# Kernel optimization log

Measured on AMD Instinct MI355X. Metric: run time of the kernel, lower is better.

Reference implementation:

```python
import jax, jax.numpy as jnp
import numpy as np

TEMPERATURE = 3.0
SINKHORN_ITERS = 20
NOISE_SCALE = 1.0
EPS = 1e-20


def setup_inputs() -> dict:
    key = jax.random.key(0)
    k1, k2, k3 = jax.random.split(key, 3)
    x = jax.random.normal(k1, (524288, 128), dtype=jnp.float32)
    logits = jax.random.normal(k2, (128, 128), dtype=jnp.float32)
    u = jax.random.uniform(k3, (128, 128), dtype=jnp.float32)
    return {"x": x, "logits": logits, "u": u}


def reference(x, logits, u):
    # Gumbel noise from uniform sample (matches sample_gumbel)
    gumbel = -jnp.log(-jnp.log(u + EPS) + EPS) * NOISE_SCALE
    log_alpha = (logits + gumbel) / TEMPERATURE
    log_alpha = jnp.clip(log_alpha, -10.0, 10.0)
    A = jnp.exp(log_alpha)
    # Sinkhorn: alternate row / column normalization (fixed 20 iters)
    for _ in range(SINKHORN_ITERS):
        A = A / jnp.sum(A, axis=1, keepdims=True)
        A = A / jnp.sum(A, axis=0, keepdims=True)
    P = jnp.nan_to_num(A, nan=0.0, posinf=1.0, neginf=0.0)
    # [batch, num_inputs] @ [num_inputs, num_leaves]
    return x @ P.T
```

## Files before the change

kernel.cpp:

```cpp
#include <hip/hip_runtime.h>
#include <hip/hip_bf16.h>

typedef _Float16 half8 __attribute__((ext_vector_type(8)));
typedef float floatx4 __attribute__((ext_vector_type(4)));

__global__ __launch_bounds__(128, 1) void sinkhorn128(
    const float* __restrict__ logits, const float* __restrict__ u,
    _Float16* __restrict__ Pout) {
    __shared__ float sA[128 * 129];
    __shared__ alignas(16) float sVec[128];
    const int i = threadIdx.x;

    float a0[128];
    float a0t[128];

    #pragma unroll
    for (int j = 0; j < 128; ++j) {
        float lg = logits[i * 128 + j];
        float uu = u[i * 128 + j];
        float g  = -logf(-logf(uu + 1e-20f) + 1e-20f);
        float la = (lg + g) / 3.0f;
        la = fminf(10.0f, fmaxf(-10.0f, la));
        float a = expf(la);
        a0[j] = a;
        sA[i * 129 + j] = a;
    }
    sVec[i] = 1.0f;
    __syncthreads();
    #pragma unroll
    for (int j = 0; j < 128; ++j) a0t[j] = sA[j * 129 + i];

    float ri = 1.0f;
    for (int it = 0; it < 20; ++it) {
        float s0 = 0.f, s1 = 0.f, s2 = 0.f, s3 = 0.f;
        #pragma unroll
        for (int j = 0; j < 128; j += 4) {
            float4 c4 = *reinterpret_cast<const float4*>(&sVec[j]);
            s0 = fmaf(a0[j + 0], c4.x, s0);
            s1 = fmaf(a0[j + 1], c4.y, s1);
            s2 = fmaf(a0[j + 2], c4.z, s2);
            s3 = fmaf(a0[j + 3], c4.w, s3);
        }
        ri = 1.0f / ((s0 + s1) + (s2 + s3));
        __syncthreads();
        sVec[i] = ri;
        __syncthreads();
        s0 = s1 = s2 = s3 = 0.f;
        #pragma unroll
        for (int j = 0; j < 128; j += 4) {
            float4 r4 = *reinterpret_cast<const float4*>(&sVec[j]);
            s0 = fmaf(a0t[j + 0], r4.x, s0);
            s1 = fmaf(a0t[j + 1], r4.y, s1);
            s2 = fmaf(a0t[j + 2], r4.z, s2);
            s3 = fmaf(a0t[j + 3], r4.w, s3);
        }
        float ci = 1.0f / ((s0 + s1) + (s2 + s3));
        __syncthreads();
        sVec[i] = ci;
        __syncthreads();
    }

    #pragma unroll
    for (int j = 0; j < 128; j += 2) {
        union { _Float16 h[2]; unsigned int w; } pk;
        pk.h[0] = (_Float16)(ri * a0[j + 0] * sVec[j + 0]);
        pk.h[1] = (_Float16)(ri * a0[j + 1] * sVec[j + 1]);
        reinterpret_cast<unsigned int*>(Pout)[(i * 128 + j) >> 1] = pk.w;
    }
}

__global__ __launch_bounds__(256, 2) void streamMatmul(
    const float* __restrict__ x, const _Float16* __restrict__ P,
    float* __restrict__ out) {
    const int lane = threadIdx.x & 63;
    const int wv   = threadIdx.x >> 6;
    const int gw   = blockIdx.x * 4 + wv;
    const int r    = lane & 15;
    const int q    = lane >> 4;

    half8 Bf[4][8];
    #pragma unroll
    for (int ks = 0; ks < 4; ++ks)
        #pragma unroll
        for (int nt = 0; nt < 8; ++nt)
            Bf[ks][nt] = *reinterpret_cast<const half8*>(
                P + (nt * 16 + r) * 128 + ks * 32 + q * 8);

    const long baseRow = (long)gw * 256;
    for (int t = 0; t < 16; ++t) {
        const long m0 = baseRow + t * 16;
        const float* xp = x + (m0 + r) * 128 + q * 8;

        floatx4 xa[4][2];
        #pragma unroll
        for (int ks = 0; ks < 4; ++ks) {
            xa[ks][0] = __builtin_nontemporal_load(
                reinterpret_cast<const floatx4*>(xp + ks * 32));
            xa[ks][1] = __builtin_nontemporal_load(
                reinterpret_cast<const floatx4*>(xp + ks * 32 + 4));
        }

        floatx4 acc[8];
        #pragma unroll
        for (int nt = 0; nt < 8; ++nt) acc[nt] = (floatx4){0.f, 0.f, 0.f, 0.f};

        #pragma unroll
        for (int ks = 0; ks < 4; ++ks) {
            half8 ahi, alo;
            #pragma unroll
            for (int jj = 0; jj < 8; ++jj) {
                float f = (jj < 4) ? xa[ks][0][jj] : xa[ks][1][jj - 4];
                _Float16 h = (_Float16)f;
                ahi[jj] = h;
                alo[jj] = (_Float16)(f - (float)h);
            }
            #pragma unroll
            for (int nt = 0; nt < 8; ++nt) {
                acc[nt] = __builtin_amdgcn_mfma_f32_16x16x32_f16(
                    ahi, Bf[ks][nt], acc[nt], 0, 0, 0);
                acc[nt] = __builtin_amdgcn_mfma_f32_16x16x32_f16(
                    alo, Bf[ks][nt], acc[nt], 0, 0, 0);
            }
        }

        float* op = out + (m0 + q * 4) * 128 + r;
        #pragma unroll
        for (int nt = 0; nt < 8; ++nt)
            #pragma unroll
            for (int rr = 0; rr < 4; ++rr)
                __builtin_nontemporal_store(acc[nt][rr], op + rr * 128 + nt * 16);
    }
}

extern "C" void kernel_launch(void* const* d_in, const int* in_sizes, int n_in,
                              void* d_out, int out_size, void* d_ws, size_t ws_size,
                              hipStream_t stream) {
    (void)in_sizes; (void)n_in; (void)out_size; (void)ws_size;
    const float* x      = (const float*)d_in[0];
    const float* logits = (const float*)d_in[1];
    const float* u      = (const float*)d_in[2];
    float* out          = (float*)d_out;
    _Float16* P         = (_Float16*)d_ws;

    sinkhorn128<<<1, 128, 0, stream>>>(logits, u, P);
    streamMatmul<<<512, 256, 0, stream>>>(x, P, out);
}
```

Measured before the change: 534.0 us.

## Split Sinkhorn row/column work across 256 threads and double-buffer x loads

The Sinkhorn kernel now runs 256 threads, with one half owning rows and the other half owning columns, so each thread keeps a single 128-float register array instead of two. The initialisation is spread across all threads and uses fast __logf/__expf intrinsics. The matmul kernel prefetches the next 16-row x tile into a second register buffer while computing the current one, to hide global load latency. Costs are higher register pressure in the matmul kernel and slightly less accurate transcendentals in the Sinkhorn prologue.

```diff
diff --git a/kernel.cpp b/kernel.cpp
--- a/kernel.cpp
+++ b/kernel.cpp
@@ -4,68 +4,79 @@
 typedef _Float16 half8 __attribute__((ext_vector_type(8)));
 typedef float floatx4 __attribute__((ext_vector_type(4)));
 
-__global__ __launch_bounds__(128, 1) void sinkhorn128(
+__global__ __launch_bounds__(256, 1) void sinkhorn128(
     const float* __restrict__ logits, const float* __restrict__ u,
     _Float16* __restrict__ Pout) {
     __shared__ float sA[128 * 129];
-    __shared__ alignas(16) float sVec[128];
-    const int i = threadIdx.x;
+    __shared__ alignas(16) float sC[128];
+    __shared__ alignas(16) float sR[128];
+    const int t = threadIdx.x;
+    const bool isRow = t < 128;
+    const int idx = t & 127;
 
-    float a0[128];
-    float a0t[128];
+    #pragma unroll 4
+    for (int j = 0; j < 64; ++j) {
+        const int f = t * 64 + j;
+        float lg = logits[f];
+        float uu = u[f];
+        float g  = -__logf(-__logf(uu + 1e-20f) + 1e-20f);
+        float la = (lg + g) * (1.0f / 3.0f);
+        la = fminf(10.0f, fmaxf(-10.0f, la));
+        sA[(f >> 7) * 129 + (f & 127)] = __expf(la);
+    }
+    if (t < 128) sC[t] = 1.0f;
+    __syncthreads();
 
-    #pragma unroll
-    for (int j = 0; j < 128; ++j) {
-        float lg = logits[i * 128 + j];
-        float uu = u[i * 128 + j];
-        float g  = -logf(-logf(uu + 1e-20f) + 1e-20f);
-        float la = (lg + g) / 3.0f;
-        la = fminf(10.0f, fmaxf(-10.0f, la));
-        float a = expf(la);
-        a0[j] = a;
-        sA[i * 129 + j] = a;
+    float av[128];
+    if (isRow) {
+        #pragma unroll
+        for (int j = 0; j < 128; ++j) av[j] = sA[idx * 129 + j];
+    } else {
+        #pragma unroll
+        for (int j = 0; j < 128; ++j) av[j] = sA[j * 129 + idx];
     }
-    sVec[i] = 1.0f;
-    __syncthreads();
-    #pragma unroll
-    for (int j = 0; j < 128; ++j) a0t[j] = sA[j * 129 + i];
 
     float ri = 1.0f;
+    #pragma unroll 1
     for (int it = 0; it < 20; ++it) {
-        float s0 = 0.f, s1 = 0.f, s2 = 0.f, s3 = 0.f;
-        #pragma unroll
-        for (int j = 0; j < 128; j += 4) {
-            float4 c4 = *reinterpret_cast<const float4*>(&sVec[j]);
-            s0 = fmaf(a0[j + 0], c4.x, s0);
-            s1 = fmaf(a0[j + 1], c4.y, s1);
-            s2 = fmaf(a0[j + 2], c4.z, s2);
-            s3 = fmaf(a0[j + 3], c4.w, s3);
+        if (isRow) {
+            float s0 = 0.f, s1 = 0.f, s2 = 0.f, s3 = 0.f;
+            #pragma unroll
+            for (int j = 0; j < 128; j += 4) {
+                float4 c4 = *reinterpret_cast<const float4*>(&sC[j]);
+                s0 = fmaf(av[j + 0], c4.x, s0);
+                s1 = fmaf(av[j + 1], c4.y, s1);
+                s2 = fmaf(av[j + 2], c4.z, s2);
+                s3 = fmaf(av[j + 3], c4.w, s3);
+            }
+            ri = 1.0f / ((s0 + s1) + (s2 + s3));
         }
-        ri = 1.0f / ((s0 + s1) + (s2 + s3));
         __syncthreads();
-        sVec[i] = ri;
+        if (isRow) sR[idx] = ri;
         __syncthreads();
-        s0 = s1 = s2 = s3 = 0.f;
-        #pragma unroll
-        for (int j = 0; j < 128; j += 4) {
-            float4 r4 = *reinterpret_cast<const float4*>(&sVec[j]);
-            s0 = fmaf(a0t[j + 0], r4.x, s0);
-            s1 = fmaf(a0t[j + 1], r4.y, s1);
-            s2 = fmaf(a0t[j + 2], r4.z, s2);
-            s3 = fmaf(a0t[j + 3], r4.w, s3);
+        if (!isRow) {
+            float s0 = 0.f, s1 = 0.f, s2 = 0.f, s3 = 0.f;
+            #pragma unroll
+            for (int j = 0; j < 128; j += 4) {
+                float4 r4 = *reinterpret_cast<const float4*>(&sR[j]);
+                s0 = fmaf(av[j + 0], r4.x, s0);
+                s1 = fmaf(av[j + 1], r4.y, s1);
+                s2 = fmaf(av[j + 2], r4.z, s2);
+                s3 = fmaf(av[j + 3], r4.w, s3);
+            }
+            sC[idx] = 1.0f / ((s0 + s1) + (s2 + s3));
         }
-        float ci = 1.0f / ((s0 + s1) + (s2 + s3));
-        __syncthreads();
-        sVec[i] = ci;
         __syncthreads();
     }
 
-    #pragma unroll
-    for (int j = 0; j < 128; j += 2) {
-        union { _Float16 h[2]; unsigned int w; } pk;
-        pk.h[0] = (_Float16)(ri * a0[j + 0] * sVec[j + 0]);
-        pk.h[1] = (_Float16)(ri * a0[j + 1] * sVec[j + 1]);
-        reinterpret_cast<unsigned int*>(Pout)[(i * 128 + j) >> 1] = pk.w;
+    if (isRow) {
+        #pragma unroll
+        for (int j = 0; j < 128; j += 2) {
+            union { _Float16 h[2]; unsigned int w; } pk;
+            pk.h[0] = (_Float16)(ri * av[j + 0] * sC[j + 0]);
+            pk.h[1] = (_Float16)(ri * av[j + 1] * sC[j + 1]);
+            reinterpret_cast<unsigned int*>(Pout)[(idx * 128 + j) >> 1] = pk.w;
+        }
     }
 }
 
@@ -87,11 +98,12 @@
                 P + (nt * 16 + r) * 128 + ks * 32 + q * 8);
 
     const long baseRow = (long)gw * 256;
-    for (int t = 0; t < 16; ++t) {
-        const long m0 = baseRow + t * 16;
-        const float* xp = x + (m0 + r) * 128 + q * 8;
+    const float* xbase = x + (baseRow + r) * 128 + q * 8;
 
-        floatx4 xa[4][2];
+    floatx4 xa0[4][2], xa1[4][2];
+
+    auto issue = [&](int t, floatx4 (&xa)[4][2]) {
+        const float* xp = xbase + (long)t * (16 * 128);
         #pragma unroll
         for (int ks = 0; ks < 4; ++ks) {
             xa[ks][0] = __builtin_nontemporal_load(
@@ -99,11 +111,12 @@
             xa[ks][1] = __builtin_nontemporal_load(
                 reinterpret_cast<const floatx4*>(xp + ks * 32 + 4));
         }
+    };
 
+    auto compute_store = [&](int t, floatx4 (&xa)[4][2]) {
         floatx4 acc[8];
         #pragma unroll
         for (int nt = 0; nt < 8; ++nt) acc[nt] = (floatx4){0.f, 0.f, 0.f, 0.f};
-
         #pragma unroll
         for (int ks = 0; ks < 4; ++ks) {
             half8 ahi, alo;
@@ -122,13 +135,22 @@
                     alo, Bf[ks][nt], acc[nt], 0, 0, 0);
             }
         }
-
-        float* op = out + (m0 + q * 4) * 128 + r;
+        float* op = out + (baseRow + t * 16 + q * 4) * 128 + r;
         #pragma unroll
         for (int nt = 0; nt < 8; ++nt)
             #pragma unroll
             for (int rr = 0; rr < 4; ++rr)
-                __builtin_nontemporal_store(acc[nt][rr], op + rr * 128 + nt * 16);
+                __builtin_nontemporal_store(acc[nt][rr],
+                                            op + rr * 128 + nt * 16);
+    };
+
+    issue(0, xa0);
+    #pragma unroll 1
+    for (int t = 0; t < 16; t += 2) {
+        issue(t + 1, xa1);
+        compute_store(t, xa0);
+        if (t + 2 < 16) issue(t + 2, xa0);
+        compute_store(t + 1, xa1);
     }
 }
 
@@ -142,6 +164,6 @@
     float* out          = (float*)d_out;
     _Float16* P         = (_Float16*)d_ws;
 
-    sinkhorn128<<<1, 128, 0, stream>>>(logits, u, P);
+    sinkhorn128<<<1, 256, 0, stream>>>(logits, u, P);
     streamMatmul<<<512, 256, 0, stream>>>(x, P, out);
 }
```

New measurement: 536.1 us. Within noise of the previous version (+0.4%).
